# Performance work log

Measured on AMD Instinct MI355X. Metric: run time of the kernel, lower is better.

Reference implementation:

```python
import jax, jax.numpy as jnp
import numpy as np

N = 50000      # nodes
E = 800000     # edges (avg degree 16)
D = 64         # node feature dim
DE = 32        # edge feature dim
H = 256        # MLP hidden dim


def setup_inputs() -> dict:
    key = jax.random.key(0)
    k0, k1, k2, k3, k4 = jax.random.split(key, 5)
    x = jax.random.normal(k0, (N, D), dtype=jnp.float32)
    edge_index = jax.random.randint(k1, (2, E), 0, N)
    edge_attr = jax.random.normal(k2, (E, DE), dtype=jnp.float32)
    fan_in1 = 2 * D + DE  # 160
    W1 = jax.random.normal(k3, (fan_in1, H), dtype=jnp.float32) / np.float32(np.sqrt(fan_in1))
    b1 = jnp.zeros((H,), dtype=jnp.float32)
    W2 = jax.random.normal(k4, (H, D), dtype=jnp.float32) / np.float32(np.sqrt(H))
    b2 = jnp.zeros((D,), dtype=jnp.float32)
    return {"x": x, "edge_index": edge_index, "edge_attr": edge_attr,
            "W1": W1, "b1": b1, "W2": W2, "b2": b2}


def reference(x, edge_index, edge_attr, W1, b1, W2, b2):
    row, col = edge_index[0], edge_index[1]
    # gather endpoint features + edge features -> [E, 2D+DE]
    feats = jnp.concatenate([x[row], x[col], edge_attr], axis=-1)
    # MLP: Linear -> ReLU -> Linear
    h = jax.nn.relu(feats @ W1 + b1)          # [E, H]
    out = h @ W2 + b2                          # [E, D]
    # scatter-max aggregate by source node (row), dim_size = N
    agg = jax.ops.segment_max(out, row, num_segments=N)  # [N, D]
    # PyG's old scatter_('max') zero-fills empty slots
    agg = jnp.where(jnp.isneginf(agg), jnp.float32(0.0), agg)
    return (agg, out)
```

## Files before the change

kernel.cpp:

```cpp
#include <hip/hip_runtime.h>
#include <hip/hip_bf16.h>
#include <math.h>

#define NNODES 50000
#define NEDGES 800000
#define CHUNKS (NEDGES / 32)
#define NBLK 256
#define GWAVES (NBLK * 16)

using short8 = __attribute__((ext_vector_type(8))) short;
using f32x4  = __attribute__((ext_vector_type(4))) float;
using f32x16 = __attribute__((ext_vector_type(16))) float;
using u32x4  = __attribute__((ext_vector_type(4))) unsigned;

__device__ __forceinline__ short f2b(float v) {
    return __builtin_bit_cast(short, __float2bfloat16(v));
}
__device__ __forceinline__ unsigned cvt2(float a, float b) {
    return (unsigned)(unsigned short)f2b(a) | ((unsigned)(unsigned short)f2b(b) << 16);
}

__global__ void prep_all(const float* __restrict__ x, short* __restrict__ xb,
                         const float* __restrict__ W1, const float* __restrict__ W2,
                         short* __restrict__ wpk, const int* __restrict__ ei,
                         unsigned* __restrict__ cnt)
{
    int b = blockIdx.x;
    if (b < 3125) {
        int i = b * 256 + threadIdx.x;
        float4 v = reinterpret_cast<const float4*>(x)[i];
        short4 o;
        o.x = f2b(v.x); o.y = f2b(v.y); o.z = f2b(v.z); o.w = f2b(v.w);
        reinterpret_cast<short4*>(xb)[i] = o;
    } else if (b < 6250) {
        int e = (b - 3125) * 256 + threadIdx.x;
        atomicAdd(&cnt[ei[e]], 1u);
    } else {
        int i = (b - 6250) * 256 + threadIdx.x;
        if (i < 40960) {
            int k = i >> 8, n = i & 255;
            int lane = (n & 31) + (((k >> 3) & 1) << 5);
            wpk[(((n >> 5) * 10 + (k >> 4)) * 64 + lane) * 8 + (k & 7)] = f2b(W1[i]);
        }
        if (i < 16384) {
            int k = i >> 6, n = i & 63;
            int lane = (n & 31) + (((k >> 3) & 1) << 5);
            wpk[40960 + (((n >> 5) * 16 + (k >> 4)) * 64 + lane) * 8 + (k & 7)] = f2b(W2[i]);
        }
    }
}

__global__ __launch_bounds__(1024)
void csr_scan1(const unsigned* __restrict__ cnt, unsigned* __restrict__ offs,
               unsigned* __restrict__ bsum) {
    __shared__ unsigned sbuf[1024];
    int t = threadIdx.x, i = blockIdx.x * 1024 + t;
    unsigned v = (i < NNODES) ? cnt[i] : 0u;
    sbuf[t] = v;
    __syncthreads();
    for (int off = 1; off < 1024; off <<= 1) {
        unsigned add = (t >= off) ? sbuf[t - off] : 0u;
        __syncthreads();
        sbuf[t] += add;
        __syncthreads();
    }
    if (i < NNODES) offs[i] = sbuf[t];
    if (t == 1023) bsum[blockIdx.x] = sbuf[1023];
}

__global__ void csr_scan2(unsigned* __restrict__ bsum) {
    int t = threadIdx.x;
    unsigned v = (t < 49) ? bsum[t] : 0u;
    unsigned orig = v;
    for (int off = 1; off < 64; off <<= 1) {
        unsigned n = __shfl_up(v, off, 64);
        if (t >= off) v += n;
    }
    if (t < 49) bsum[t] = v - orig;
}

__global__ __launch_bounds__(1024)
void csr_scan3(const unsigned* __restrict__ cnt, unsigned* __restrict__ offs,
               const unsigned* __restrict__ bsum) {
    int i = blockIdx.x * 1024 + threadIdx.x;
    if (i < NNODES)       offs[i] = offs[i] - cnt[i] + bsum[blockIdx.x];
    else if (i == NNODES) offs[i] = NEDGES;
}

__global__ void csr_place(const int* __restrict__ ei, const unsigned* __restrict__ offs,
                          unsigned* __restrict__ cur, unsigned* __restrict__ elist) {
    int e = blockIdx.x * 256 + threadIdx.x;
    if (e < NEDGES) {
        int r = ei[e];
        unsigned p = offs[r] + atomicAdd(&cur[r], 1u);
        elist[p] = (unsigned)e;
    }
}

__global__ __launch_bounds__(1024)
void edgeconv_main(const short* __restrict__ xb, const int* __restrict__ ei,
                   const float* __restrict__ ea, const short* __restrict__ wpk,
                   const float* __restrict__ b1, const float* __restrict__ b2,
                   float* __restrict__ outbuf)
{
    __shared__ short wlds[57344];

    for (int i = threadIdx.x; i < 7168; i += 1024)
        reinterpret_cast<short8*>(wlds)[i] = reinterpret_cast<const short8*>(wpk)[i];
    __syncthreads();

    const short* w1s = wlds;
    const short* w2s = wlds + 40960;
    const int lane = threadIdx.x & 63;
    const int wave = threadIdx.x >> 6;
    const int l32 = lane & 31, hi = lane >> 5;
    const int gw = blockIdx.x * 16 + wave;

    int r = 0, cc = 0;
    if (gw < CHUNKS) {
        int e0 = gw * 32 + l32;
        r  = ei[e0];
        cc = ei[NEDGES + e0];
    }

    for (int c = gw; c < CHUNKS; c += GWAVES) {
        const int e = c * 32 + l32;

        int cn = c + GWAVES;
        int r_n = 0, cc_n = 0;
        if (cn < CHUNKS) {
            int e1 = cn * 32 + l32;
            r_n  = ei[e1];
            cc_n = ei[NEDGES + e1];
        }

        short8 fx[10];
        #pragma unroll
        for (int ks = 0; ks < 4; ++ks)
            fx[ks] = *reinterpret_cast<const short8*>(xb + r * 64 + ks * 16 + hi * 8);
        #pragma unroll
        for (int ks = 0; ks < 4; ++ks)
            fx[4 + ks] = *reinterpret_cast<const short8*>(xb + cc * 64 + ks * 16 + hi * 8);
        #pragma unroll
        for (int ks = 0; ks < 2; ++ks) {
            const float4* p = reinterpret_cast<const float4*>(ea + (size_t)e * 32 + ks * 16 + hi * 8);
            float4 a = p[0], b = p[1];
            u32x4 uu;
            uu[0] = cvt2(a.x, a.y); uu[1] = cvt2(a.z, a.w);
            uu[2] = cvt2(b.x, b.y); uu[3] = cvt2(b.z, b.w);
            fx[8 + ks] = __builtin_bit_cast(short8, uu);
        }

        f32x16 acc2[2];
        #pragma unroll
        for (int t2 = 0; t2 < 2; ++t2)
            #pragma unroll
            for (int g = 0; g < 4; ++g) {
                float4 bb = *reinterpret_cast<const float4*>(b2 + t2 * 32 + g * 8 + hi * 4);
                acc2[t2][g * 4 + 0] = bb.x; acc2[t2][g * 4 + 1] = bb.y;
                acc2[t2][g * 4 + 2] = bb.z; acc2[t2][g * 4 + 3] = bb.w;
            }

        #pragma unroll 2
        for (int t = 0; t < 8; ++t) {
            f32x16 acc1;
            #pragma unroll
            for (int g = 0; g < 4; ++g) {
                float4 bb = *reinterpret_cast<const float4*>(b1 + t * 32 + g * 8 + hi * 4);
                acc1[g * 4 + 0] = bb.x; acc1[g * 4 + 1] = bb.y;
                acc1[g * 4 + 2] = bb.z; acc1[g * 4 + 3] = bb.w;
            }
            #pragma unroll
            for (int ks = 0; ks < 10; ++ks) {
                short8 wf = *reinterpret_cast<const short8*>(
                    w1s + ((t * 10 + ks) * 64 + lane) * 8);
                acc1 = __builtin_amdgcn_mfma_f32_32x32x16_bf16(wf, fx[ks], acc1, 0, 0, 0);
            }
            #pragma unroll
            for (int ksl = 0; ksl < 2; ++ksl) {
                int q0 = ksl * 8;
                unsigned D0 = cvt2(fmaxf(acc1[q0 + 0], 0.f), fmaxf(acc1[q0 + 1], 0.f));
                unsigned D1 = cvt2(fmaxf(acc1[q0 + 2], 0.f), fmaxf(acc1[q0 + 3], 0.f));
                unsigned D2 = cvt2(fmaxf(acc1[q0 + 4], 0.f), fmaxf(acc1[q0 + 5], 0.f));
                unsigned D3 = cvt2(fmaxf(acc1[q0 + 6], 0.f), fmaxf(acc1[q0 + 7], 0.f));
                asm("v_permlane32_swap_b32 %0, %1" : "+v"(D0), "+v"(D2));
                asm("v_permlane32_swap_b32 %0, %1" : "+v"(D1), "+v"(D3));
                u32x4 bu; bu[0] = D0; bu[1] = D1; bu[2] = D2; bu[3] = D3;
                short8 hb = __builtin_bit_cast(short8, bu);

                int ks2 = t * 2 + ksl;
                short8 w20 = *reinterpret_cast<const short8*>(w2s + (ks2 * 64 + lane) * 8);
                short8 w21 = *reinterpret_cast<const short8*>(w2s + ((16 + ks2) * 64 + lane) * 8);
                acc2[0] = __builtin_amdgcn_mfma_f32_32x32x16_bf16(w20, hb, acc2[0], 0, 0, 0);
                acc2[1] = __builtin_amdgcn_mfma_f32_32x32x16_bf16(w21, hb, acc2[1], 0, 0, 0);
            }
        }

        #pragma unroll
        for (int t2 = 0; t2 < 2; ++t2)
            #pragma unroll
            for (int g = 0; g < 4; ++g) {
                f32x4 v;
                v[0] = acc2[t2][g * 4 + 0]; v[1] = acc2[t2][g * 4 + 1];
                v[2] = acc2[t2][g * 4 + 2]; v[3] = acc2[t2][g * 4 + 3];
                *reinterpret_cast<f32x4*>(outbuf + (size_t)e * 64 + t2 * 32 + g * 8 + hi * 4) = v;
            }

        r = r_n; cc = cc_n;
    }
}

__global__ __launch_bounds__(256)
void agg_list(const unsigned* __restrict__ offs, const unsigned* __restrict__ elist,
              const float* __restrict__ outbuf, float* __restrict__ agg)
{
    const int wave = threadIdx.x >> 6, lane = threadIdx.x & 63;
    const int node = blockIdx.x * 4 + wave;
    if (node >= NNODES) return;
    const unsigned s = offs[node], eend = offs[node + 1];
    float m0 = -INFINITY, m1 = -INFINITY, m2 = -INFINITY, m3 = -INFINITY;
    unsigned p = s;
    for (; p + 4 <= eend; p += 4) {
        float a = outbuf[(size_t)elist[p + 0] * 64 + lane];
        float b = outbuf[(size_t)elist[p + 1] * 64 + lane];
        float c = outbuf[(size_t)elist[p + 2] * 64 + lane];
        float d = outbuf[(size_t)elist[p + 3] * 64 + lane];
        m0 = fmaxf(m0, a); m1 = fmaxf(m1, b);
        m2 = fmaxf(m2, c); m3 = fmaxf(m3, d);
    }
    for (; p < eend; ++p) m0 = fmaxf(m0, outbuf[(size_t)elist[p] * 64 + lane]);
    float m = fmaxf(fmaxf(m0, m1), fmaxf(m2, m3));
    agg[(size_t)node * 64 + lane] = (s == eend) ? 0.0f : m;
}

extern "C" void kernel_launch(void* const* d_in, const int* in_sizes, int n_in,
                              void* d_out, int out_size, void* d_ws, size_t ws_size,
                              hipStream_t stream)
{
    const float* x  = (const float*)d_in[0];
    const int*   ei = (const int*)d_in[1];
    const float* ea = (const float*)d_in[2];
    const float* W1 = (const float*)d_in[3];
    const float* b1 = (const float*)d_in[4];
    const float* W2 = (const float*)d_in[5];
    const float* b2 = (const float*)d_in[6];

    float* aggp = (float*)d_out;
    float* outp = aggp + (size_t)NNODES * 64;

    short*    xb   = (short*)d_ws;
    short*    wpk  = (short*)((char*)d_ws + 6400000);
    unsigned* meta = (unsigned*)((char*)d_ws + 6514688);
    unsigned* cnt   = meta;
    unsigned* cur   = meta + 50000;
    unsigned* offs  = meta + 100000;
    unsigned* bsum  = meta + 150016;
    unsigned* elist = meta + 150144;

    (void)hipMemsetAsync(cnt, 0, 100000 * sizeof(unsigned), stream);
    prep_all<<<6410, 256, 0, stream>>>(x, xb, W1, W2, wpk, ei, cnt);
    csr_scan1<<<49, 1024, 0, stream>>>(cnt, offs, bsum);
    csr_scan2<<<1, 64, 0, stream>>>(bsum);
    csr_scan3<<<49, 1024, 0, stream>>>(cnt, offs, bsum);
    csr_place<<<NEDGES / 256, 256, 0, stream>>>(ei, offs, cur, elist);
    edgeconv_main<<<NBLK, 1024, 0, stream>>>(xb, ei, ea, wpk, b1, b2, outp);
    agg_list<<<(NNODES + 3) / 4, 256, 0, stream>>>(offs, elist, outp, aggp);
}
```

Before: 310.2 us.

## Process two 32-edge groups per wave to reuse W1/W2 LDS fragments

Each wave now handles 64 edges per chunk as two 32-edge groups, so every W1 and W2 fragment read from LDS feeds two MFMAs instead of one. Blocks shrink to 512 threads with launch bounds of 2 blocks per CU, and the hidden-tile loop is no longer unrolled, to keep register pressure manageable. The aggregation loop is unrolled to 8 independent max accumulators for more memory-level parallelism. The cost is roughly doubled accumulator and fragment register usage, which may cut occupancy or cause spills. The grid stays at 256 blocks, so only half as many waves are resident overall.

```diff
diff --git a/kernel.cpp b/kernel.cpp
--- a/kernel.cpp
+++ b/kernel.cpp
@@ -4,9 +4,9 @@
 
 #define NNODES 50000
 #define NEDGES 800000
-#define CHUNKS (NEDGES / 32)
+#define CHUNKS (NEDGES / 64)
 #define NBLK 256
-#define GWAVES (NBLK * 16)
+#define GWAVES (NBLK * 8)
 
 using short8 = __attribute__((ext_vector_type(8))) short;
 using f32x4  = __attribute__((ext_vector_type(4))) float;
@@ -97,7 +97,7 @@
     }
 }
 
-__global__ __launch_bounds__(1024)
+__global__ __launch_bounds__(512, 2)
 void edgeconv_main(const short* __restrict__ xb, const int* __restrict__ ei,
                    const float* __restrict__ ea, const short* __restrict__ wpk,
                    const float* __restrict__ b1, const float* __restrict__ b2,
@@ -105,7 +105,7 @@
 {
     __shared__ short wlds[57344];
 
-    for (int i = threadIdx.x; i < 7168; i += 1024)
+    for (int i = threadIdx.x; i < 7168; i += 512)
         reinterpret_cast<short8*>(wlds)[i] = reinterpret_cast<const short8*>(wpk)[i];
     __syncthreads();
 
@@ -114,99 +114,115 @@
     const int lane = threadIdx.x & 63;
     const int wave = threadIdx.x >> 6;
     const int l32 = lane & 31, hi = lane >> 5;
-    const int gw = blockIdx.x * 16 + wave;
-
-    int r = 0, cc = 0;
-    if (gw < CHUNKS) {
-        int e0 = gw * 32 + l32;
-        r  = ei[e0];
-        cc = ei[NEDGES + e0];
+    const int gw = blockIdx.x * 8 + wave;
+
+    int r0 = 0, r1 = 0, c0 = 0, c1 = 0;
+    {
+        int ea0 = gw * 64 + l32, ea1 = gw * 64 + 32 + l32;
+        r0 = ei[ea0]; c0 = ei[NEDGES + ea0];
+        r1 = ei[ea1]; c1 = ei[NEDGES + ea1];
     }
 
     for (int c = gw; c < CHUNKS; c += GWAVES) {
-        const int e = c * 32 + l32;
-
         int cn = c + GWAVES;
-        int r_n = 0, cc_n = 0;
+        int r0n = 0, r1n = 0, c0n = 0, c1n = 0;
         if (cn < CHUNKS) {
-            int e1 = cn * 32 + l32;
-            r_n  = ei[e1];
-            cc_n = ei[NEDGES + e1];
-        }
-
-        short8 fx[10];
+            int ea0 = cn * 64 + l32, ea1 = cn * 64 + 32 + l32;
+            r0n = ei[ea0]; c0n = ei[NEDGES + ea0];
+            r1n = ei[ea1]; c1n = ei[NEDGES + ea1];
+        }
+
+        short8 fx[2][10];
         #pragma unroll
-        for (int ks = 0; ks < 4; ++ks)
-            fx[ks] = *reinterpret_cast<const short8*>(xb + r * 64 + ks * 16 + hi * 8);
-        #pragma unroll
-        for (int ks = 0; ks < 4; ++ks)
-            fx[4 + ks] = *reinterpret_cast<const short8*>(xb + cc * 64 + ks * 16 + hi * 8);
-        #pragma unroll
-        for (int ks = 0; ks < 2; ++ks) {
-            const float4* p = reinterpret_cast<const float4*>(ea + (size_t)e * 32 + ks * 16 + hi * 8);
-            float4 a = p[0], b = p[1];
-            u32x4 uu;
-            uu[0] = cvt2(a.x, a.y); uu[1] = cvt2(a.z, a.w);
-            uu[2] = cvt2(b.x, b.y); uu[3] = cvt2(b.z, b.w);
-            fx[8 + ks] = __builtin_bit_cast(short8, uu);
-        }
-
-        f32x16 acc2[2];
+        for (int g = 0; g < 2; ++g) {
+            const int rr = g ? r1 : r0, cg = g ? c1 : c0;
+            const int e = c * 64 + g * 32 + l32;
+            #pragma unroll
+            for (int ks = 0; ks < 4; ++ks)
+                fx[g][ks] = *reinterpret_cast<const short8*>(xb + rr * 64 + ks * 16 + hi * 8);
+            #pragma unroll
+            for (int ks = 0; ks < 4; ++ks)
+                fx[g][4 + ks] = *reinterpret_cast<const short8*>(xb + cg * 64 + ks * 16 + hi * 8);
+            #pragma unroll
+            for (int ks = 0; ks < 2; ++ks) {
+                const float4* p = reinterpret_cast<const float4*>(ea + (size_t)e * 32 + ks * 16 + hi * 8);
+                float4 a = p[0], b = p[1];
+                u32x4 uu;
+                uu[0] = cvt2(a.x, a.y); uu[1] = cvt2(a.z, a.w);
+                uu[2] = cvt2(b.x, b.y); uu[3] = cvt2(b.z, b.w);
+                fx[g][8 + ks] = __builtin_bit_cast(short8, uu);
+            }
+        }
+
+        f32x16 acc2[2][2];
         #pragma unroll
         for (int t2 = 0; t2 < 2; ++t2)
             #pragma unroll
-            for (int g = 0; g < 4; ++g) {
-                float4 bb = *reinterpret_cast<const float4*>(b2 + t2 * 32 + g * 8 + hi * 4);
-                acc2[t2][g * 4 + 0] = bb.x; acc2[t2][g * 4 + 1] = bb.y;
-                acc2[t2][g * 4 + 2] = bb.z; acc2[t2][g * 4 + 3] = bb.w;
-            }
-
-        #pragma unroll 2
+            for (int gg = 0; gg < 4; ++gg) {
+                float4 bb = *reinterpret_cast<const float4*>(b2 + t2 * 32 + gg * 8 + hi * 4);
+                #pragma unroll
+                for (int g = 0; g < 2; ++g) {
+                    acc2[t2][g][gg * 4 + 0] = bb.x; acc2[t2][g][gg * 4 + 1] = bb.y;
+                    acc2[t2][g][gg * 4 + 2] = bb.z; acc2[t2][g][gg * 4 + 3] = bb.w;
+                }
+            }
+
+        #pragma unroll 1
         for (int t = 0; t < 8; ++t) {
-            f32x16 acc1;
-            #pragma unroll
-            for (int g = 0; g < 4; ++g) {
-                float4 bb = *reinterpret_cast<const float4*>(b1 + t * 32 + g * 8 + hi * 4);
-                acc1[g * 4 + 0] = bb.x; acc1[g * 4 + 1] = bb.y;
-                acc1[g * 4 + 2] = bb.z; acc1[g * 4 + 3] = bb.w;
+            f32x16 acc1[2];
+            #pragma unroll
+            for (int gg = 0; gg < 4; ++gg) {
+                float4 bb = *reinterpret_cast<const float4*>(b1 + t * 32 + gg * 8 + hi * 4);
+                #pragma unroll
+                for (int g = 0; g < 2; ++g) {
+                    acc1[g][gg * 4 + 0] = bb.x; acc1[g][gg * 4 + 1] = bb.y;
+                    acc1[g][gg * 4 + 2] = bb.z; acc1[g][gg * 4 + 3] = bb.w;
+                }
             }
             #pragma unroll
             for (int ks = 0; ks < 10; ++ks) {
                 short8 wf = *reinterpret_cast<const short8*>(
                     w1s + ((t * 10 + ks) * 64 + lane) * 8);
-                acc1 = __builtin_amdgcn_mfma_f32_32x32x16_bf16(wf, fx[ks], acc1, 0, 0, 0);
+                acc1[0] = __builtin_amdgcn_mfma_f32_32x32x16_bf16(wf, fx[0][ks], acc1[0], 0, 0, 0);
+                acc1[1] = __builtin_amdgcn_mfma_f32_32x32x16_bf16(wf, fx[1][ks], acc1[1], 0, 0, 0);
             }
             #pragma unroll
             for (int ksl = 0; ksl < 2; ++ksl) {
-                int q0 = ksl * 8;
-                unsigned D0 = cvt2(fmaxf(acc1[q0 + 0], 0.f), fmaxf(acc1[q0 + 1], 0.f));
-                unsigned D1 = cvt2(fmaxf(acc1[q0 + 2], 0.f), fmaxf(acc1[q0 + 3], 0.f));
-                unsigned D2 = cvt2(fmaxf(acc1[q0 + 4], 0.f), fmaxf(acc1[q0 + 5], 0.f));
-                unsigned D3 = cvt2(fmaxf(acc1[q0 + 6], 0.f), fmaxf(acc1[q0 + 7], 0.f));
-                asm("v_permlane32_swap_b32 %0, %1" : "+v"(D0), "+v"(D2));
-                asm("v_permlane32_swap_b32 %0, %1" : "+v"(D1), "+v"(D3));
-                u32x4 bu; bu[0] = D0; bu[1] = D1; bu[2] = D2; bu[3] = D3;
-                short8 hb = __builtin_bit_cast(short8, bu);
-
                 int ks2 = t * 2 + ksl;
                 short8 w20 = *reinterpret_cast<const short8*>(w2s + (ks2 * 64 + lane) * 8);
                 short8 w21 = *reinterpret_cast<const short8*>(w2s + ((16 + ks2) * 64 + lane) * 8);
-                acc2[0] = __builtin_amdgcn_mfma_f32_32x32x16_bf16(w20, hb, acc2[0], 0, 0, 0);
-                acc2[1] = __builtin_amdgcn_mfma_f32_32x32x16_bf16(w21, hb, acc2[1], 0, 0, 0);
+                #pragma unroll
+                for (int g = 0; g < 2; ++g) {
+                    int q0 = ksl * 8;
+                    unsigned D0 = cvt2(fmaxf(acc1[g][q0 + 0], 0.f), fmaxf(acc1[g][q0 + 1], 0.f));
+                    unsigned D1 = cvt2(fmaxf(acc1[g][q0 + 2], 0.f), fmaxf(acc1[g][q0 + 3], 0.f));
+                    unsigned D2 = cvt2(fmaxf(acc1[g][q0 + 4], 0.f), fmaxf(acc1[g][q0 + 5], 0.f));
+                    unsigned D3 = cvt2(fmaxf(acc1[g][q0 + 6], 0.f), fmaxf(acc1[g][q0 + 7], 0.f));
+                    asm("v_permlane32_swap_b32 %0, %1" : "+v"(D0), "+v"(D2));
+                    asm("v_permlane32_swap_b32 %0, %1" : "+v"(D1), "+v"(D3));
+                    u32x4 bu; bu[0] = D0; bu[1] = D1; bu[2] = D2; bu[3] = D3;
+                    short8 hb = __builtin_bit_cast(short8, bu);
+                    acc2[0][g] = __builtin_amdgcn_mfma_f32_32x32x16_bf16(w20, hb, acc2[0][g], 0, 0, 0);
+                    acc2[1][g] = __builtin_amdgcn_mfma_f32_32x32x16_bf16(w21, hb, acc2[1][g], 0, 0, 0);
+                }
             }
         }
 
         #pragma unroll
-        for (int t2 = 0; t2 < 2; ++t2)
-            #pragma unroll
-            for (int g = 0; g < 4; ++g) {
-                f32x4 v;
-                v[0] = acc2[t2][g * 4 + 0]; v[1] = acc2[t2][g * 4 + 1];
-                v[2] = acc2[t2][g * 4 + 2]; v[3] = acc2[t2][g * 4 + 3];
-                *reinterpret_cast<f32x4*>(outbuf + (size_t)e * 64 + t2 * 32 + g * 8 + hi * 4) = v;
-            }
-
-        r = r_n; cc = cc_n;
+        for (int g = 0; g < 2; ++g) {
+            const int e = c * 64 + g * 32 + l32;
+            #pragma unroll
+            for (int t2 = 0; t2 < 2; ++t2)
+                #pragma unroll
+                for (int gg = 0; gg < 4; ++gg) {
+                    f32x4 v;
+                    v[0] = acc2[t2][g][gg * 4 + 0]; v[1] = acc2[t2][g][gg * 4 + 1];
+                    v[2] = acc2[t2][g][gg * 4 + 2]; v[3] = acc2[t2][g][gg * 4 + 3];
+                    *reinterpret_cast<f32x4*>(outbuf + (size_t)e * 64 + t2 * 32 + gg * 8 + hi * 4) = v;
+                }
+        }
+
+        r0 = r0n; r1 = r1n; c0 = c0n; c1 = c1n;
     }
 }
 
@@ -219,17 +235,23 @@
     if (node >= NNODES) return;
     const unsigned s = offs[node], eend = offs[node + 1];
     float m0 = -INFINITY, m1 = -INFINITY, m2 = -INFINITY, m3 = -INFINITY;
+    float m4 = -INFINITY, m5 = -INFINITY, m6 = -INFINITY, m7 = -INFINITY;
     unsigned p = s;
-    for (; p + 4 <= eend; p += 4) {
+    for (; p + 8 <= eend; p += 8) {
         float a = outbuf[(size_t)elist[p + 0] * 64 + lane];
         float b = outbuf[(size_t)elist[p + 1] * 64 + lane];
         float c = outbuf[(size_t)elist[p + 2] * 64 + lane];
         float d = outbuf[(size_t)elist[p + 3] * 64 + lane];
-        m0 = fmaxf(m0, a); m1 = fmaxf(m1, b);
-        m2 = fmaxf(m2, c); m3 = fmaxf(m3, d);
+        float e = outbuf[(size_t)elist[p + 4] * 64 + lane];
+        float f = outbuf[(size_t)elist[p + 5] * 64 + lane];
+        float g = outbuf[(size_t)elist[p + 6] * 64 + lane];
+        float h = outbuf[(size_t)elist[p + 7] * 64 + lane];
+        m0 = fmaxf(m0, a); m1 = fmaxf(m1, b); m2 = fmaxf(m2, c); m3 = fmaxf(m3, d);
+        m4 = fmaxf(m4, e); m5 = fmaxf(m5, f); m6 = fmaxf(m6, g); m7 = fmaxf(m7, h);
     }
     for (; p < eend; ++p) m0 = fmaxf(m0, outbuf[(size_t)elist[p] * 64 + lane]);
-    float m = fmaxf(fmaxf(m0, m1), fmaxf(m2, m3));
+    float m = fmaxf(fmaxf(fmaxf(m0, m1), fmaxf(m2, m3)),
+                    fmaxf(fmaxf(m4, m5), fmaxf(m6, m7)));
     agg[(size_t)node * 64 + lane] = (s == eend) ? 0.0f : m;
 }
 
@@ -263,6 +285,6 @@
     csr_scan2<<<1, 64, 0, stream>>>(bsum);
     csr_scan3<<<49, 1024, 0, stream>>>(cnt, offs, bsum);
     csr_place<<<NEDGES / 256, 256, 0, stream>>>(ei, offs, cur, elist);
-    edgeconv_main<<<NBLK, 1024, 0, stream>>>(xb, ei, ea, wpk, b1, b2, outp);
+    edgeconv_main<<<NBLK, 512, 0, stream>>>(xb, ei, ea, wpk, b1, b2, outp);
     agg_list<<<(NNODES + 3) / 4, 256, 0, stream>>>(offs, elist, outp, aggp);
 }
```

Result: faster. 289.6 us (median of 2 runs) (-6.6%).
